# Kernel tuning notes

Hardware: AMD Instinct MI355X
Metric: run time of the kernel (lower is better)

Reference implementation:

```python
import jax, jax.numpy as jnp
import numpy as np
import math

SPARSITY = 0.95


def _linear(x, W, b):
    # torch nn.Linear: y = x @ W.T + b, W is [out, in]
    return jnp.einsum('bsd,od->bso', x, W) + b


def setup_inputs() -> dict:
    key = jax.random.key(0)
    ks = jax.random.split(key, 11)
    B, S, D = 2, 4096, 512
    std = 1.0 / math.sqrt(D)
    inp = {
        'x': jax.random.normal(ks[0], (B, S, D), dtype=jnp.float32),
        'mask_rand': jax.random.uniform(ks[1], (B, S, S), dtype=jnp.float32),
        'Wq': jax.random.normal(ks[2], (D, D), dtype=jnp.float32) * std,
        'bq': jax.random.normal(ks[3], (D,), dtype=jnp.float32) * std,
        'Wk': jax.random.normal(ks[4], (D, D), dtype=jnp.float32) * std,
        'bk': jax.random.normal(ks[5], (D,), dtype=jnp.float32) * std,
        'Wv': jax.random.normal(ks[6], (D, D), dtype=jnp.float32) * std,
        'bv': jax.random.normal(ks[7], (D,), dtype=jnp.float32) * std,
        'Wo': jax.random.normal(ks[8], (D, D), dtype=jnp.float32) * std,
        'bo': jax.random.normal(ks[9], (D,), dtype=jnp.float32) * std,
    }
    return inp


def reference(x, mask_rand, Wq, bq, Wk, bk, Wv, bv, Wo, bo):
    B, S, D = x.shape
    Q = _linear(x, Wq, bq)
    K = _linear(x, Wk, bk)
    V = _linear(x, Wv, bv)
    scores = jnp.einsum('bqd,bkd->bqk', Q, K) / jnp.sqrt(jnp.asarray(D, x.dtype))
    keep = mask_rand > SPARSITY  # random sparsity mask
    sparse_scores = jnp.where(keep, scores, -jnp.inf)
    attn = jax.nn.softmax(sparse_scores, axis=-1)
    attn_out = jnp.einsum('bqk,bkd->bqd', attn, V)
    # faithful to torch: transpose(1,2).contiguous().view(B, S, D)
    attn_out = jnp.swapaxes(attn_out, 1, 2).reshape(B, S, D)
    return _linear(attn_out, Wo, bo)
```

## Files before the change

kernel.cpp:

```cpp
#include <hip/hip_runtime.h>
#include <hip/hip_bf16.h>
#include <math.h>

typedef __bf16 bf16_t;
typedef __attribute__((ext_vector_type(8))) __bf16 bf16x8;
typedef __attribute__((ext_vector_type(4))) float f32x4;

constexpr int B_ = 2, S_ = 4096, D_ = 512;
constexpr int BS_ = B_ * S_;
constexpr int GRID_ = 512;
constexpr int NT_ = 256;
constexpr long QKV_E  = (long)BS_ * D_;
constexpr long W_E    = (long)D_ * D_;
constexpr long MASK_N = (long)BS_ * S_;
constexpr long CVT_UNITS  = (QKV_E + 4 * W_E) / 4;
constexpr long PACK_UNITS = MASK_N / 16;
constexpr float SCALE_ = 0.044194173824159216f;

__device__ __forceinline__ void load16_lds(const bf16_t* g, bf16_t* l) {
    __builtin_amdgcn_global_load_lds(
        (const __attribute__((address_space(1))) void*)g,
        (__attribute__((address_space(3))) void*)l, 16, 0, 0);
}

__device__ __forceinline__ void dev_cvt(long u,
    const float* x, const float* Wq, const float* Wk, const float* Wv,
    const float* Wo, bf16_t* dst)
{
    const long i = u * 4;
    const float* src; long o;
    if (i < QKV_E) { src = x; o = i; }
    else {
        const long j = i - QKV_E;
        const int w = (int)(j >> 18);
        o = j & (W_E - 1);
        src = (w == 0) ? Wq : (w == 1) ? Wk : (w == 2) ? Wv : Wo;
    }
    const float4 v = *(const float4*)(src + o);
    bf16_t out[4] = {(bf16_t)v.x, (bf16_t)v.y, (bf16_t)v.z, (bf16_t)v.w};
    *(uint2*)(dst + i) = *(uint2*)out;
}

__device__ __forceinline__ void dev_pack(long u,
    const float* mask, unsigned char* bm)
{
    const long i = u * 16;
    unsigned char o[16];
#pragma unroll
    for (int c = 0; c < 4; c++) {
        const float4 v = *(const float4*)(mask + i + c * 4);
        o[c * 4 + 0] = v.x > 0.95f;
        o[c * 4 + 1] = v.y > 0.95f;
        o[c * 4 + 2] = v.z > 0.95f;
        o[c * 4 + 3] = v.w > 0.95f;
    }
    *(uint4*)(bm + i) = *(uint4*)o;
}

__device__ __forceinline__ void kloop64(
    const bf16_t* At, const bf16_t* Bt, long ldA, long ldB, int kSteps,
    bf16_t* As, bf16_t* Bs, int tid, int wr, int wc, int quad, int r16,
    f32x4 (&acc)[4][4])
{
    const int srow = tid >> 3;
    const int cg = ((tid & 7) ^ (srow & 7)) * 8;
    const bf16_t* gA = At + (long)srow * ldA + cg;
    const bf16_t* gB = Bt + (long)srow * ldB + cg;
    bf16_t* lA = As + tid * 8;
    bf16_t* lB = Bs + tid * 8;

    for (int s = 0; s < kSteps; s++) {
        const int k0 = s * 64;
#pragma unroll
        for (int rr = 0; rr < 4; rr++) {
            load16_lds(gA + (long)rr * 32 * ldA + k0, lA + rr * 2048);
            load16_lds(gB + (long)rr * 32 * ldB + k0, lB + rr * 2048);
        }
        __syncthreads();
#pragma unroll
        for (int kh = 0; kh < 2; kh++) {
            bf16x8 af[4], bfr[4];
#pragma unroll
            for (int i = 0; i < 4; i++) {
                const int row = wr * 64 + i * 16 + r16;
                af[i] = *(const bf16x8*)(As + row * 64 +
                        (((kh << 2) + quad) ^ (row & 7)) * 8);
            }
#pragma unroll
            for (int j = 0; j < 4; j++) {
                const int row = wc * 64 + j * 16 + r16;
                bfr[j] = *(const bf16x8*)(Bs + row * 64 +
                        (((kh << 2) + quad) ^ (row & 7)) * 8);
            }
#pragma unroll
            for (int i = 0; i < 4; i++)
#pragma unroll
                for (int j = 0; j < 4; j++)
                    acc[i][j] = __builtin_amdgcn_mfma_f32_16x16x32_bf16(
                        af[i], bfr[j], acc[i][j], 0, 0, 0);
        }
        __syncthreads();
    }
}

__device__ __forceinline__ void dev_qkv_tile(int t,
    const bf16_t* Xc, const bf16_t* Wqc, const bf16_t* Wkc, const bf16_t* Wvc,
    const float* bq, const float* bk, const float* bv,
    bf16_t* Q, bf16_t* Kp, bf16_t* V, char* smem, int tid)
{
    constexpr int K = 512, N = 512;
    const int xs = t % 12, y = t / 12;
    const int sel = xs >> 2;
    const bf16_t* Bw = (sel == 0) ? Wqc : (sel == 1) ? Wkc : Wvc;
    const float* bias = (sel == 0) ? bq : (sel == 1) ? bk : bv;
    bf16_t* C = (sel == 0) ? Q : (sel == 1) ? Kp : V;
    const int m0 = y * 128, n0 = (xs & 3) * 128;

    bf16_t* As = (bf16_t*)smem;
    bf16_t* Bs = As + 128 * 64;
    const int wave = tid >> 6, lane = tid & 63;
    const int quad = lane >> 4, r16 = lane & 15;
    const int wr = wave >> 1, wc = wave & 1;

    f32x4 acc[4][4] = {};
    kloop64(Xc + (long)m0 * K, Bw + (long)n0 * K, K, K, K / 64,
            As, Bs, tid, wr, wc, quad, r16, acc);

#pragma unroll
    for (int i = 0; i < 4; i++)
#pragma unroll
        for (int j = 0; j < 4; j++) {
            const int gn = n0 + wc * 64 + j * 16 + r16;
            const float bval = bias[gn];
#pragma unroll
            for (int reg = 0; reg < 4; reg++) {
                const int gm = m0 + wr * 64 + i * 16 + quad * 4 + reg;
                C[(long)gm * N + gn] = (bf16_t)(acc[i][j][reg] + bval);
            }
        }
}

__device__ __forceinline__ void dev_transpose_tile(int t,
    const bf16_t* V, bf16_t* VT, char* smem, int tid)
{
    bf16_t (*tile)[33] = (bf16_t(*)[33])smem;
    const int cx = t & 15;
    const int ry = (t >> 4) & 127;
    const int b  = t >> 11;
    const bf16_t* in = V + (long)b * S_ * D_;
    bf16_t* out = VT + (long)b * S_ * D_;
    const int r0 = ry * 32, c0 = cx * 32;
    const int tx = tid & 31, ty = tid >> 5;
#pragma unroll
    for (int i = 0; i < 4; i++)
        tile[ty + 8 * i][tx] = in[(long)(r0 + ty + 8 * i) * D_ + c0 + tx];
    __syncthreads();
#pragma unroll
    for (int i = 0; i < 4; i++)
        out[(long)(c0 + ty + 8 * i) * S_ + r0 + tx] = tile[tx][ty + 8 * i];
    __syncthreads();
}

__device__ __forceinline__ void dev_scores_tile(int t,
    const bf16_t* Q, const bf16_t* Kp, const unsigned char* bmask,
    bf16_t* SC, float* rowsum, char* smem, int tid)
{
    constexpr int S = S_, K = D_;
    const int x = t & 31;
    const int y = (t >> 5) & 31;
    const int b = t >> 10;
    const int m0 = y * 128, n0 = x * 128;

    bf16_t* As = (bf16_t*)smem;
    bf16_t* Bs = As + 128 * 64;
    const int wave = tid >> 6, lane = tid & 63;
    const int quad = lane >> 4, r16 = lane & 15;
    const int wr = wave >> 1, wc = wave & 1;

    f32x4 acc[4][4] = {};
    kloop64(Q + (long)b * S * K + (long)m0 * K,
            Kp + (long)b * S * K + (long)n0 * K, K, K, K / 64,
            As, Bs, tid, wr, wc, quad, r16, acc);

    float* wlds = (float*)smem + wave * 1024;
    const int erow = lane >> 2;
    const int ecg  = lane & 3;
    const long mbase = (long)b * S * S;

#pragma unroll
    for (int i = 0; i < 4; i++) {
#pragma unroll
        for (int j = 0; j < 4; j++)
#pragma unroll
            for (int reg = 0; reg < 4; reg++)
                wlds[(quad * 4 + reg) * 64 + j * 16 + r16] = acc[i][j][reg];
        __syncthreads();

        float v[16];
#pragma unroll
        for (int c = 0; c < 4; c++) {
            const float4 tv = *(const float4*)(wlds + erow * 64 + ecg * 16 + c * 4);
            v[c * 4 + 0] = tv.x; v[c * 4 + 1] = tv.y;
            v[c * 4 + 2] = tv.z; v[c * 4 + 3] = tv.w;
        }

        const int gm = m0 + wr * 64 + i * 16 + erow;
        const int gn = n0 + wc * 64 + ecg * 16;

        const uint4 mb = *(const uint4*)(bmask + mbase + (long)gm * S + gn);
        const unsigned char* mk = (const unsigned char*)&mb;
        float e[16];
#pragma unroll
        for (int tt = 0; tt < 16; tt++)
            e[tt] = mk[tt] ? __expf(v[tt] * SCALE_) : 0.f;

        bf16x8 o0, o1;
        float rsum = 0.f;
#pragma unroll
        for (int tt = 0; tt < 8; tt++) {
            rsum += e[tt] + e[tt + 8];
            o0[tt] = (bf16_t)e[tt];
            o1[tt] = (bf16_t)e[tt + 8];
        }
        bf16_t* cp = SC + mbase + (long)gm * S + gn;
        *(bf16x8*)cp       = o0;
        *(bf16x8*)(cp + 8) = o1;

        rsum += __shfl_xor(rsum, 1, 64);
        rsum += __shfl_xor(rsum, 2, 64);
        if (ecg == 0) atomicAdd(&rowsum[b * S + gm], rsum);
        __syncthreads();
    }
}

__device__ __forceinline__ void dev_pv_tile(int t,
    const bf16_t* VT, const bf16_t* SC, const float* rowsum,
    bf16_t* part, char* smem, int tid)
{
    constexpr int S = S_, D = D_, KS = 4;
    constexpr int KC = S / KS;
    const int x = t & 31;
    const int y = (t >> 5) & 3;
    const int z = t >> 7;
    const int b = z / KS, ks = z % KS;
    const int m0 = y * 128, n0 = x * 128;
    const int kbeg = ks * KC;

    bf16_t* As = (bf16_t*)smem;
    bf16_t* Bs = As + 128 * 64;
    const int wave = tid >> 6, lane = tid & 63;
    const int quad = lane >> 4, r16 = lane & 15;
    const int wr = wave >> 1, wc = wave & 1;

    f32x4 acc[4][4] = {};
    kloop64(VT + (long)b * D * S + (long)m0 * S + kbeg,
            SC + (long)b * S * S + (long)n0 * S + kbeg, S, S, KC / 64,
            As, Bs, tid, wr, wc, quad, r16, acc);

    const long obase = ((long)ks * B_ + b) * (long)D * S;
#pragma unroll
    for (int i = 0; i < 4; i++)
#pragma unroll
        for (int j = 0; j < 4; j++) {
            const int gn = n0 + wc * 64 + j * 16 + r16;
            const float inv = 1.f / rowsum[b * S + gn];
#pragma unroll
            for (int reg = 0; reg < 4; reg++) {
                const int gm = m0 + wr * 64 + i * 16 + quad * 4 + reg;
                part[obase + (long)gm * S + gn] = (bf16_t)(acc[i][j][reg] * inv);
            }
        }
}

__device__ __forceinline__ void dev_reduce(long u,
    const bf16_t* part, bf16_t* T)
{
    const long i = u * 4;
    float s[4] = {0.f, 0.f, 0.f, 0.f};
#pragma unroll
    for (int ks = 0; ks < 4; ks++) {
        const bf16_t* p = part + (long)ks * QKV_E + i;
#pragma unroll
        for (int tt = 0; tt < 4; tt++) s[tt] += (float)p[tt];
    }
    bf16_t o[4] = {(bf16_t)s[0], (bf16_t)s[1], (bf16_t)s[2], (bf16_t)s[3]};
    *(uint2*)(T + i) = *(uint2*)o;
}

__device__ __forceinline__ void dev_out_tile(int t,
    const bf16_t* T, const bf16_t* Woc, const float* bo, float* C,
    char* smem, int tid)
{
    constexpr int N = 512, K = 512;
    const int m0 = (t >> 2) * 128, n0 = (t & 3) * 128;

    bf16_t* As = (bf16_t*)smem;
    bf16_t* Bs = As + 128 * 64;
    const int wave = tid >> 6, lane = tid & 63;
    const int quad = lane >> 4, r16 = lane & 15;
    const int wr = wave >> 1, wc = wave & 1;

    f32x4 acc[4][4] = {};
    kloop64(T + (long)m0 * K, Woc + (long)n0 * K, K, K, K / 64,
            As, Bs, tid, wr, wc, quad, r16, acc);

#pragma unroll
    for (int i = 0; i < 4; i++)
#pragma unroll
        for (int j = 0; j < 4; j++) {
            const int gn = n0 + wc * 64 + j * 16 + r16;
            const float bval = bo[gn];
#pragma unroll
            for (int reg = 0; reg < 4; reg++) {
                const int gm = m0 + wr * 64 + i * 16 + quad * 4 + reg;
                C[(long)gm * N + gn] = acc[i][j][reg] + bval;
            }
        }
}

__global__ __launch_bounds__(256) void k_s1(
    const float* x, const float* mask, const float* Wq, const float* Wk,
    const float* Wv, const float* Wo, bf16_t* Xc, unsigned char* bmask,
    float* rowsum)
{
    const long gtid = (long)blockIdx.x * NT_ + threadIdx.x;
    for (long u = gtid; u < CVT_UNITS; u += (long)GRID_ * NT_)
        dev_cvt(u, x, Wq, Wk, Wv, Wo, Xc);
    for (long u = gtid; u < PACK_UNITS; u += (long)GRID_ * NT_)
        dev_pack(u, mask, bmask);
    if (gtid < BS_ / 4) {
        const float4 z = {0.f, 0.f, 0.f, 0.f};
        *(float4*)(rowsum + gtid * 4) = z;
    }
}

__global__ __launch_bounds__(256) void k_s2(
    const bf16_t* Xc, const float* bq, const float* bk, const float* bv,
    bf16_t* Q, bf16_t* Kp, bf16_t* V)
{
    __shared__ char smem[32768];
    const bf16_t* Wqc = Xc + QKV_E;
    for (int t = blockIdx.x; t < 768; t += GRID_)
        dev_qkv_tile(t, Xc, Wqc, Wqc + W_E, Wqc + 2 * W_E,
                     bq, bk, bv, Q, Kp, V, smem, threadIdx.x);
}

__global__ __launch_bounds__(256) void k_s3(
    const bf16_t* V, bf16_t* VT, const bf16_t* Q, const bf16_t* Kp,
    const unsigned char* bmask, bf16_t* SC, float* rowsum)
{
    __shared__ char smem[32768];
    for (int t = blockIdx.x; t < 4096; t += GRID_)
        dev_transpose_tile(t, V, VT, smem, threadIdx.x);
    for (int t = blockIdx.x; t < 2048; t += GRID_)
        dev_scores_tile(t, Q, Kp, bmask, SC, rowsum, smem, threadIdx.x);
}

__global__ __launch_bounds__(256) void k_s4(
    const bf16_t* VT, const bf16_t* SC, const float* rowsum, bf16_t* part)
{
    __shared__ char smem[32768];
    for (int t = blockIdx.x; t < 1024; t += GRID_)
        dev_pv_tile(t, VT, SC, rowsum, part, smem, threadIdx.x);
}

__global__ __launch_bounds__(256) void k_s5(const bf16_t* part, bf16_t* T)
{
    const long gtid = (long)blockIdx.x * NT_ + threadIdx.x;
    for (long u = gtid; u < QKV_E / 4; u += (long)GRID_ * NT_)
        dev_reduce(u, part, T);
}

__global__ __launch_bounds__(256) void k_s6(
    const bf16_t* T, const bf16_t* Xc, const float* bo, float* C)
{
    __shared__ char smem[32768];
    const bf16_t* Woc = Xc + QKV_E + 3 * W_E;
    dev_out_tile(blockIdx.x, T, Woc, bo, C, smem, threadIdx.x);
}

extern "C" void kernel_launch(void* const* d_in, const int* in_sizes, int n_in,
                              void* d_out, int out_size, void* d_ws, size_t ws_size,
                              hipStream_t stream)
{
    const float* x    = (const float*)d_in[0];
    const float* mask = (const float*)d_in[1];
    const float* Wq   = (const float*)d_in[2];
    const float* bq   = (const float*)d_in[3];
    const float* Wk   = (const float*)d_in[4];
    const float* bk   = (const float*)d_in[5];
    const float* Wv   = (const float*)d_in[6];
    const float* bv   = (const float*)d_in[7];
    const float* Wo   = (const float*)d_in[8];
    const float* bo   = (const float*)d_in[9];
    float* outp = (float*)d_out;

    char* ws = (char*)d_ws;
    bf16_t* SC = (bf16_t*)ws;   ws += (long)BS_ * S_ * 2;
    bf16_t* VT = (bf16_t*)ws;   ws += QKV_E * 2;
    bf16_t* Q  = (bf16_t*)ws;   ws += QKV_E * 2;
    bf16_t* Kp = (bf16_t*)ws;   ws += QKV_E * 2;
    bf16_t* V  = (bf16_t*)ws;   ws += QKV_E * 2;
    bf16_t* Xc = (bf16_t*)ws;   ws += (QKV_E + 4 * W_E) * 2;
    float* rowsum = (float*)ws; ws += (long)BS_ * 4;
    unsigned char* bmask = (unsigned char*)ws;
    bf16_t* part = (bf16_t*)ws;

    dim3 blk(NT_);
    k_s1<<<dim3(GRID_), blk, 0, stream>>>(x, mask, Wq, Wk, Wv, Wo,
                                          Xc, bmask, rowsum);
    k_s2<<<dim3(GRID_), blk, 0, stream>>>(Xc, bq, bk, bv, Q, Kp, V);
    k_s3<<<dim3(GRID_), blk, 0, stream>>>(V, VT, Q, Kp, bmask, SC, rowsum);
    k_s4<<<dim3(GRID_), blk, 0, stream>>>(VT, SC, rowsum, part);
    k_s5<<<dim3(GRID_), blk, 0, stream>>>(part, V);
    k_s6<<<dim3(256), blk, 0, stream>>>(V, Xc, bo, outp);
}
```

Before: 430.7 us.

## Compute V transposed in QKV GEMM, halve PV split-K, fuse reduce into output GEMM

```diff
diff --git a/kernel.cpp b/kernel.cpp
--- a/kernel.cpp
+++ b/kernel.cpp
@@ -106,15 +106,11 @@
 __device__ __forceinline__ void dev_qkv_tile(int t,
     const bf16_t* Xc, const bf16_t* Wqc, const bf16_t* Wkc, const bf16_t* Wvc,
     const float* bq, const float* bk, const float* bv,
-    bf16_t* Q, bf16_t* Kp, bf16_t* V, char* smem, int tid)
-{
-    constexpr int K = 512, N = 512;
-    const int xs = t % 12, y = t / 12;
-    const int sel = xs >> 2;
-    const bf16_t* Bw = (sel == 0) ? Wqc : (sel == 1) ? Wkc : Wvc;
-    const float* bias = (sel == 0) ? bq : (sel == 1) ? bk : bv;
-    bf16_t* C = (sel == 0) ? Q : (sel == 1) ? Kp : V;
-    const int m0 = y * 128, n0 = (xs & 3) * 128;
+    bf16_t* Q, bf16_t* Kp, bf16_t* VT, char* smem, int tid)
+{
+    constexpr int K = 512;
+    const int sel = t >> 8;
+    const int tt  = t & 255;
 
     bf16_t* As = (bf16_t*)smem;
     bf16_t* Bs = As + 128 * 64;
@@ -123,42 +119,46 @@
     const int wr = wave >> 1, wc = wave & 1;
 
     f32x4 acc[4][4] = {};
-    kloop64(Xc + (long)m0 * K, Bw + (long)n0 * K, K, K, K / 64,
-            As, Bs, tid, wr, wc, quad, r16, acc);
-
-#pragma unroll
-    for (int i = 0; i < 4; i++)
-#pragma unroll
-        for (int j = 0; j < 4; j++) {
-            const int gn = n0 + wc * 64 + j * 16 + r16;
-            const float bval = bias[gn];
-#pragma unroll
-            for (int reg = 0; reg < 4; reg++) {
-                const int gm = m0 + wr * 64 + i * 16 + quad * 4 + reg;
-                C[(long)gm * N + gn] = (bf16_t)(acc[i][j][reg] + bval);
-            }
-        }
-}
-
-__device__ __forceinline__ void dev_transpose_tile(int t,
-    const bf16_t* V, bf16_t* VT, char* smem, int tid)
-{
-    bf16_t (*tile)[33] = (bf16_t(*)[33])smem;
-    const int cx = t & 15;
-    const int ry = (t >> 4) & 127;
-    const int b  = t >> 11;
-    const bf16_t* in = V + (long)b * S_ * D_;
-    bf16_t* out = VT + (long)b * S_ * D_;
-    const int r0 = ry * 32, c0 = cx * 32;
-    const int tx = tid & 31, ty = tid >> 5;
-#pragma unroll
-    for (int i = 0; i < 4; i++)
-        tile[ty + 8 * i][tx] = in[(long)(r0 + ty + 8 * i) * D_ + c0 + tx];
-    __syncthreads();
-#pragma unroll
-    for (int i = 0; i < 4; i++)
-        out[(long)(c0 + ty + 8 * i) * S_ + r0 + tx] = tile[tx][ty + 8 * i];
-    __syncthreads();
+
+    if (sel < 2) {
+        const int m0 = (tt >> 2) * 128;
+        const int n0 = (tt & 3) * 128;
+        const bf16_t* Bw = sel ? Wkc : Wqc;
+        const float* bias = sel ? bk : bq;
+        bf16_t* C = sel ? Kp : Q;
+        kloop64(Xc + (long)m0 * K, Bw + (long)n0 * K, K, K, K / 64,
+                As, Bs, tid, wr, wc, quad, r16, acc);
+#pragma unroll
+        for (int i = 0; i < 4; i++)
+#pragma unroll
+            for (int j = 0; j < 4; j++) {
+                const int gn = n0 + wc * 64 + j * 16 + r16;
+                const float bval = bias[gn];
+#pragma unroll
+                for (int reg = 0; reg < 4; reg++) {
+                    const int gm = m0 + wr * 64 + i * 16 + quad * 4 + reg;
+                    C[(long)gm * 512 + gn] = (bf16_t)(acc[i][j][reg] + bval);
+                }
+            }
+    } else {
+        const int m0 = (tt & 3) * 128;
+        const int n0 = (tt >> 2) * 128;
+        kloop64(Wvc + (long)m0 * K, Xc + (long)n0 * K, K, K, K / 64,
+                As, Bs, tid, wr, wc, quad, r16, acc);
+#pragma unroll
+        for (int i = 0; i < 4; i++)
+#pragma unroll
+            for (int j = 0; j < 4; j++) {
+                const int gn = n0 + wc * 64 + j * 16 + r16;
+                const int b = gn >> 12, q = gn & 4095;
+#pragma unroll
+                for (int reg = 0; reg < 4; reg++) {
+                    const int gm = m0 + wr * 64 + i * 16 + quad * 4 + reg;
+                    VT[(long)b * D_ * S_ + (long)gm * S_ + q] =
+                        (bf16_t)(acc[i][j][reg] + bv[gm]);
+                }
+            }
+    }
 }
 
 __device__ __forceinline__ void dev_scores_tile(int t,
@@ -182,7 +182,7 @@
             Kp + (long)b * S * K + (long)n0 * K, K, K, K / 64,
             As, Bs, tid, wr, wc, quad, r16, acc);
 
-    float* wlds = (float*)smem + wave * 1024;
+    float* wlds = (float*)smem + wave * 1088;
     const int erow = lane >> 2;
     const int ecg  = lane & 3;
     const long mbase = (long)b * S * S;
@@ -193,13 +193,13 @@
         for (int j = 0; j < 4; j++)
 #pragma unroll
             for (int reg = 0; reg < 4; reg++)
-                wlds[(quad * 4 + reg) * 64 + j * 16 + r16] = acc[i][j][reg];
+                wlds[(quad * 4 + reg) * 68 + j * 16 + r16] = acc[i][j][reg];
         __syncthreads();
 
         float v[16];
 #pragma unroll
         for (int c = 0; c < 4; c++) {
-            const float4 tv = *(const float4*)(wlds + erow * 64 + ecg * 16 + c * 4);
+            const float4 tv = *(const float4*)(wlds + erow * 68 + ecg * 16 + c * 4);
             v[c * 4 + 0] = tv.x; v[c * 4 + 1] = tv.y;
             v[c * 4 + 2] = tv.z; v[c * 4 + 3] = tv.w;
         }
@@ -237,12 +237,12 @@
     const bf16_t* VT, const bf16_t* SC, const float* rowsum,
     bf16_t* part, char* smem, int tid)
 {
-    constexpr int S = S_, D = D_, KS = 4;
-    constexpr int KC = S / KS;
+    constexpr int S = S_, D = D_;
+    constexpr int KC = S / 2;
     const int x = t & 31;
     const int y = (t >> 5) & 3;
     const int z = t >> 7;
-    const int b = z / KS, ks = z % KS;
+    const int b = z >> 1, ks = z & 1;
     const int m0 = y * 128, n0 = x * 128;
     const int kbeg = ks * KC;
 
@@ -272,23 +272,8 @@
         }
 }
 
-__device__ __forceinline__ void dev_reduce(long u,
-    const bf16_t* part, bf16_t* T)
-{
-    const long i = u * 4;
-    float s[4] = {0.f, 0.f, 0.f, 0.f};
-#pragma unroll
-    for (int ks = 0; ks < 4; ks++) {
-        const bf16_t* p = part + (long)ks * QKV_E + i;
-#pragma unroll
-        for (int tt = 0; tt < 4; tt++) s[tt] += (float)p[tt];
-    }
-    bf16_t o[4] = {(bf16_t)s[0], (bf16_t)s[1], (bf16_t)s[2], (bf16_t)s[3]};
-    *(uint2*)(T + i) = *(uint2*)o;
-}
-
 __device__ __forceinline__ void dev_out_tile(int t,
-    const bf16_t* T, const bf16_t* Woc, const float* bo, float* C,
+    const bf16_t* part, const bf16_t* Woc, const float* bo, float* C,
     char* smem, int tid)
 {
     constexpr int N = 512, K = 512;
@@ -300,9 +285,54 @@
     const int quad = lane >> 4, r16 = lane & 15;
     const int wr = wave >> 1, wc = wave & 1;
 
+    const int srow = tid >> 3;
+    const int cg = ((tid & 7) ^ (srow & 7)) * 8;
+    const bf16_t* gA0 = part + (long)(m0 + srow) * K + cg;
+    const bf16_t* gA1 = gA0 + QKV_E;
+    const bf16_t* gB  = Woc + (long)(n0 + srow) * K + cg;
+    bf16_t* lA = As + tid * 8;
+    bf16_t* lB = Bs + tid * 8;
+
     f32x4 acc[4][4] = {};
-    kloop64(T + (long)m0 * K, Woc + (long)n0 * K, K, K, K / 64,
-            As, Bs, tid, wr, wc, quad, r16, acc);
+
+    for (int s = 0; s < K / 64; s++) {
+        const int k0 = s * 64;
+#pragma unroll
+        for (int rr = 0; rr < 4; rr++) {
+            const bf16x8 a0 = *(const bf16x8*)(gA0 + (long)rr * 32 * K + k0);
+            const bf16x8 a1 = *(const bf16x8*)(gA1 + (long)rr * 32 * K + k0);
+            bf16x8 sm;
+#pragma unroll
+            for (int e = 0; e < 8; e++)
+                sm[e] = (bf16_t)((float)a0[e] + (float)a1[e]);
+            *(bf16x8*)(lA + rr * 2048) = sm;
+            load16_lds(gB + (long)rr * 32 * K + k0, lB + rr * 2048);
+        }
+        __syncthreads();
+#pragma unroll
+        for (int kh = 0; kh < 2; kh++) {
+            bf16x8 af[4], bfr[4];
+#pragma unroll
+            for (int i = 0; i < 4; i++) {
+                const int row = wr * 64 + i * 16 + r16;
+                af[i] = *(const bf16x8*)(As + row * 64 +
+                        (((kh << 2) + quad) ^ (row & 7)) * 8);
+            }
+#pragma unroll
+            for (int j = 0; j < 4; j++) {
+                const int row = wc * 64 + j * 16 + r16;
+                bfr[j] = *(const bf16x8*)(Bs + row * 64 +
+                        (((kh << 2) + quad) ^ (row & 7)) * 8);
+            }
+#pragma unroll
+            for (int i = 0; i < 4; i++)
+#pragma unroll
+                for (int j = 0; j < 4; j++)
+                    acc[i][j] = __builtin_amdgcn_mfma_f32_16x16x32_bf16(
+                        af[i], bfr[j], acc[i][j], 0, 0, 0);
+        }
+        __syncthreads();
+    }
 
 #pragma unroll
     for (int i = 0; i < 4; i++)
@@ -336,22 +366,20 @@
 
 __global__ __launch_bounds__(256) void k_s2(
     const bf16_t* Xc, const float* bq, const float* bk, const float* bv,
-    bf16_t* Q, bf16_t* Kp, bf16_t* V)
+    bf16_t* Q, bf16_t* Kp, bf16_t* VT)
 {
     __shared__ char smem[32768];
     const bf16_t* Wqc = Xc + QKV_E;
     for (int t = blockIdx.x; t < 768; t += GRID_)
         dev_qkv_tile(t, Xc, Wqc, Wqc + W_E, Wqc + 2 * W_E,
-                     bq, bk, bv, Q, Kp, V, smem, threadIdx.x);
+                     bq, bk, bv, Q, Kp, VT, smem, threadIdx.x);
 }
 
 __global__ __launch_bounds__(256) void k_s3(
-    const bf16_t* V, bf16_t* VT, const bf16_t* Q, const bf16_t* Kp,
-    const unsigned char* bmask, bf16_t* SC, float* rowsum)
+    const bf16_t* Q, const bf16_t* Kp, const unsigned char* bmask,
+    bf16_t* SC, float* rowsum)
 {
     __shared__ char smem[32768];
-    for (int t = blockIdx.x; t < 4096; t += GRID_)
-        dev_transpose_tile(t, V, VT, smem, threadIdx.x);
     for (int t = blockIdx.x; t < 2048; t += GRID_)
         dev_scores_tile(t, Q, Kp, bmask, SC, rowsum, smem, threadIdx.x);
 }
@@ -360,23 +388,15 @@
     const bf16_t* VT, const bf16_t* SC, const float* rowsum, bf16_t* part)
 {
     __shared__ char smem[32768];
-    for (int t = blockIdx.x; t < 1024; t += GRID_)
-        dev_pv_tile(t, VT, SC, rowsum, part, smem, threadIdx.x);
-}
-
-__global__ __launch_bounds__(256) void k_s5(const bf16_t* part, bf16_t* T)
-{
-    const long gtid = (long)blockIdx.x * NT_ + threadIdx.x;
-    for (long u = gtid; u < QKV_E / 4; u += (long)GRID_ * NT_)
-        dev_reduce(u, part, T);
+    dev_pv_tile(blockIdx.x, VT, SC, rowsum, part, smem, threadIdx.x);
 }
 
 __global__ __launch_bounds__(256) void k_s6(
-    const bf16_t* T, const bf16_t* Xc, const float* bo, float* C)
+    const bf16_t* part, const bf16_t* Xc, const float* bo, float* C)
 {
     __shared__ char smem[32768];
     const bf16_t* Woc = Xc + QKV_E + 3 * W_E;
-    dev_out_tile(blockIdx.x, T, Woc, bo, C, smem, threadIdx.x);
+    dev_out_tile(blockIdx.x, part, Woc, bo, C, smem, threadIdx.x);
 }
 
 extern "C" void kernel_launch(void* const* d_in, const int* in_sizes, int n_in,
@@ -400,7 +420,6 @@
     bf16_t* VT = (bf16_t*)ws;   ws += QKV_E * 2;
     bf16_t* Q  = (bf16_t*)ws;   ws += QKV_E * 2;
     bf16_t* Kp = (bf16_t*)ws;   ws += QKV_E * 2;
-    bf16_t* V  = (bf16_t*)ws;   ws += QKV_E * 2;
     bf16_t* Xc = (bf16_t*)ws;   ws += (QKV_E + 4 * W_E) * 2;
     float* rowsum = (float*)ws; ws += (long)BS_ * 4;
     unsigned char* bmask = (unsigned char*)ws;
@@ -409,9 +428,8 @@
     dim3 blk(NT_);
     k_s1<<<dim3(GRID_), blk, 0, stream>>>(x, mask, Wq, Wk, Wv, Wo,
                                           Xc, bmask, rowsum);
-    k_s2<<<dim3(GRID_), blk, 0, stream>>>(Xc, bq, bk, bv, Q, Kp, V);
-    k_s3<<<dim3(GRID_), blk, 0, stream>>>(V, VT, Q, Kp, bmask, SC, rowsum);
+    k_s2<<<dim3(GRID_), blk, 0, stream>>>(Xc, bq, bk, bv, Q, Kp, VT);
+    k_s3<<<dim3(GRID_), blk, 0, stream>>>(Q, Kp, bmask, SC, rowsum);
     k_s4<<<dim3(GRID_), blk, 0, stream>>>(VT, SC, rowsum, part);
-    k_s5<<<dim3(GRID_), blk, 0, stream>>>(part, V);
-    k_s6<<<dim3(256), blk, 0, stream>>>(V, Xc, bo, outp);
-}
+    k_s6<<<dim3(256), blk, 0, stream>>>(part, Xc, bo, outp);
+}
```

After: 370.8 us. 1.16x faster.
